# Optimization experiments

Measured on AMD Instinct MI355X. Metric: run time of the kernel, lower is better.

The kernel has to match this reference:

```python
import jax, jax.numpy as jnp
import numpy as np

H = 2048
NH = 16
DH = H // NH
EPS = 1e-05


def setup_inputs() -> dict:
    key = jax.random.key(0)
    ks = jax.random.split(key, 12)
    B, S, A = 4, 2048, 512
    s = 1.0 / np.sqrt(H)
    inp = {
        "hidden_states": jax.random.normal(ks[0], (B, S, H), jnp.float32),
        "audio_tokens": jax.random.normal(ks[1], (B, A, H), jnp.float32),
        "attention_mask": jax.random.randint(ks[2], (B, A), 0, 2).astype(jnp.float32),
        "Wq": jax.random.normal(ks[3], (H, H), jnp.float32) * s,
        "bq": jnp.zeros((H,), jnp.float32),
        "Wk": jax.random.normal(ks[4], (H, H), jnp.float32) * s,
        "bk": jnp.zeros((H,), jnp.float32),
        "Wv": jax.random.normal(ks[5], (H, H), jnp.float32) * s,
        "bv": jnp.zeros((H,), jnp.float32),
        "Wo": jax.random.normal(ks[6], (H, H), jnp.float32) * s,
        "bo": jnp.zeros((H,), jnp.float32),
        "gamma": jnp.ones((H,), jnp.float32),
        "beta": jnp.zeros((H,), jnp.float32),
    }
    return inp


def reference(hidden_states, audio_tokens, attention_mask,
              Wq, bq, Wk, bk, Wv, bv, Wo, bo, gamma, beta):
    B, S, _ = hidden_states.shape
    A = audio_tokens.shape[1]
    # projections (weights stored [in, out])
    q = (hidden_states @ Wq + bq).reshape(B, S, NH, DH)
    k = (audio_tokens @ Wk + bk).reshape(B, A, NH, DH)
    v = (audio_tokens @ Wv + bv).reshape(B, A, NH, DH)
    # scores: [B, NH, S, A]
    scores = jnp.einsum('bqhd,bkhd->bhqk', q, k) / np.sqrt(DH)
    scores = scores + attention_mask[:, None, None, :] * -10000.0
    probs = jax.nn.softmax(scores, axis=-1)
    # context: [B, S, NH, DH] -> [B, S, H]
    ctx = jnp.einsum('bhqk,bkhd->bqhd', probs, v).reshape(B, S, H)
    out = ctx @ Wo + bo
    # residual + LayerNorm
    x = out + hidden_states
    mu = jnp.mean(x, axis=-1, keepdims=True)
    var = jnp.mean(jnp.square(x - mu), axis=-1, keepdims=True)
    return (x - mu) * jax.lax.rsqrt(var + EPS) * gamma + beta
```

## Files before the change

### kernel.cpp

```cpp
#include <hip/hip_runtime.h>

#define HDIM 2048
#define NHEAD 16
#define DHEAD 128
#define BATCH 4
#define SEQ 2048
#define AUD 512

typedef unsigned short u16;
typedef unsigned int u32;
typedef __bf16 bf16_t;
typedef bf16_t bf16x8 __attribute__((ext_vector_type(8)));
typedef short short8 __attribute__((ext_vector_type(8)));
typedef float f32x4 __attribute__((ext_vector_type(4)));

typedef const __attribute__((address_space(1))) u32 gas_u32;
typedef __attribute__((address_space(3))) u32 las_u32;

__device__ __forceinline__ float b2f(u16 h) {
  union { u32 u; float f; } v; v.u = ((u32)h) << 16; return v.f;
}
__device__ __forceinline__ u16 f2b(float f) {
  union { float f; u32 u; } v; v.f = f;
  u32 r = (v.u + 0x7FFFu + ((v.u >> 16) & 1u)) >> 16;
  return (u16)r;
}

__global__ __launch_bounds__(256) void cvt2_k(const float* __restrict__ s0,
                                              u16* __restrict__ d0, int n0,
                                              const float* __restrict__ s1,
                                              u16* __restrict__ d1, int n1) {
  int i = blockIdx.x * 256 + threadIdx.x;
  const float* src; u16* dst; int j;
  if (i < n0) { src = s0; dst = d0; j = i; }
  else { j = i - n0; if (j >= n1) return; src = s1; dst = d1; }
  const float4* s4 = (const float4*)src;
  float4 a = s4[2 * j], b = s4[2 * j + 1];
  short8 o;
  o[0] = (short)f2b(a.x); o[1] = (short)f2b(a.y);
  o[2] = (short)f2b(a.z); o[3] = (short)f2b(a.w);
  o[4] = (short)f2b(b.x); o[5] = (short)f2b(b.y);
  o[6] = (short)f2b(b.z); o[7] = (short)f2b(b.w);
  *(short8*)(dst + (size_t)j * 8) = o;
}

__global__ __launch_bounds__(256) void transpose4_k(
    const float* __restrict__ Wq, const float* __restrict__ Wk,
    const float* __restrict__ Wv, const float* __restrict__ Wo,
    u16* __restrict__ dst4) {
  const float* src = (blockIdx.z == 0) ? Wq
                   : (blockIdx.z == 1) ? Wk
                   : (blockIdx.z == 2) ? Wv : Wo;
  u16* dst = dst4 + (size_t)blockIdx.z * HDIM * HDIM;
  __shared__ float tile[32][33];
  int tx = threadIdx.x, ty = threadIdx.y;
  int x = blockIdx.x * 32 + tx;
  int y0 = blockIdx.y * 32;
#pragma unroll
  for (int j = 0; j < 32; j += 8)
    tile[ty + j][tx] = src[(size_t)(y0 + ty + j) * HDIM + x];
  __syncthreads();
  int x2 = y0 + tx;
  int y2 = blockIdx.x * 32;
#pragma unroll
  for (int j = 0; j < 32; j += 8)
    dst[(size_t)(y2 + ty + j) * HDIM + x2] = f2b(tile[tx][ty + j]);
}

__global__ __launch_bounds__(256) void gemm_bt(
    const u16* __restrict__ A, int lda,
    const u16* __restrict__ Bt, int ldb,
    void* __restrict__ Cv, int ldc,
    const float* __restrict__ bias, float alpha, int M, int N, int K, int cmode) {
  __shared__ u16 As[128 * 32];
  __shared__ u16 Bs[128 * 32];

  int lane = threadIdx.x & 63;
  int wave = threadIdx.x >> 6;
  int gdx = gridDim.x;
  int id = blockIdx.y * gdx + blockIdx.x;
  int cpx = (gdx * gridDim.y) >> 3;
  int sid = (id & 7) * cpx + (id >> 3);
  int m0 = (sid / gdx) * 128;
  int n0 = (sid % gdx) * 128;
  int wm = (wave & 1) * 64;
  int wn = (wave >> 1) * 64;
  int row16 = lane & 15;
  int quad = lane >> 4;

  int sr = (lane >> 2);
  int sc = (lane & 3) * 8;

  f32x4 acc[4][4];
#pragma unroll
  for (int i = 0; i < 4; i++)
#pragma unroll
    for (int j = 0; j < 4; j++) acc[i][j] = (f32x4){0.f, 0.f, 0.f, 0.f};

  for (int k0 = 0; k0 < K; k0 += 32) {
#pragma unroll
    for (int t = 0; t < 2; t++) {
      int chunk = wave * 2 + t;
      int r = chunk * 16 + sr;
      const u16* ga = A + (size_t)(m0 + r) * lda + k0 + sc;
      const u16* gb = Bt + (size_t)(n0 + r) * ldb + k0 + sc;
      __builtin_amdgcn_global_load_lds((gas_u32*)ga, (las_u32*)(As + chunk * 512), 16, 0, 0);
      __builtin_amdgcn_global_load_lds((gas_u32*)gb, (las_u32*)(Bs + chunk * 512), 16, 0, 0);
    }
    __syncthreads();

    short8 af[4], bf[4];
#pragma unroll
    for (int mt = 0; mt < 4; mt++)
      af[mt] = *(const short8*)(As + (wm + mt * 16 + row16) * 32 + quad * 8);
#pragma unroll
    for (int nt = 0; nt < 4; nt++)
      bf[nt] = *(const short8*)(Bs + (wn + nt * 16 + row16) * 32 + quad * 8);
#pragma unroll
    for (int mt = 0; mt < 4; mt++)
#pragma unroll
      for (int nt = 0; nt < 4; nt++)
        acc[mt][nt] = __builtin_amdgcn_mfma_f32_16x16x32_bf16(
            __builtin_bit_cast(bf16x8, af[mt]), __builtin_bit_cast(bf16x8, bf[nt]),
            acc[mt][nt], 0, 0, 0);
    __syncthreads();
  }

#pragma unroll
  for (int nt = 0; nt < 4; nt++) {
    int nn = n0 + wn + nt * 16 + row16;
    float bv = bias ? bias[nn] : 0.f;
#pragma unroll
    for (int mt = 0; mt < 4; mt++) {
#pragma unroll
      for (int r = 0; r < 4; r++) {
        int mm = m0 + wm + mt * 16 + quad * 4 + r;
        float val = (acc[mt][nt][r] + bv) * alpha;
        if (cmode == 2) {
          ((float*)Cv)[(size_t)mm * ldc + nn] = val;
        } else if (cmode == 1) {
          int bb = mm >> 9, aa = mm & 511;
          int hh = nn >> 7, dd = nn & 127;
          ((u16*)Cv)[((size_t)((bb * 16 + hh) * 128 + dd)) * 512 + aa] = f2b(val);
        } else {
          ((u16*)Cv)[(size_t)mm * ldc + nn] = f2b(val);
        }
      }
    }
  }
}

__global__ __launch_bounds__(512, 2) void gemm_ring(
    const u16* __restrict__ A, int lda,
    const u16* __restrict__ Bt, int ldb,
    void* __restrict__ Cv, int ldc,
    const float* __restrict__ bias, float alpha, int K, int cmode) {
  __shared__ u16 As[3][256 * 64];
  __shared__ u16 Bs[3][128 * 64];

  int tid = threadIdx.x;
  int lane = tid & 63, wave = tid >> 6;
  int wr = wave >> 1, wc = wave & 1;
  int row16 = lane & 15, quad = lane >> 4;
  int swr = (row16 & 7) << 3;

  int gdx = gridDim.x;
  int id = blockIdx.y * gdx + blockIdx.x;
  int cpx = (gdx * gridDim.y) >> 3;
  int sid = (id & 7) * cpx + (id >> 3);
  int n0 = (sid % gdx) * 128;
  int m0 = (sid / gdx) * 256;

  f32x4 acc[4][4];
#pragma unroll
  for (int i = 0; i < 4; i++)
#pragma unroll
    for (int j = 0; j < 4; j++) acc[i][j] = (f32x4){0.f, 0.f, 0.f, 0.f};

  auto stage = [&](int slot, int k0) {
#pragma unroll
    for (int l = 0; l < 4; l++) {
      int d = l * 512 + tid;
      int row = d >> 3;
      int csw = ((d & 7) ^ (row & 7)) << 3;
      __builtin_amdgcn_global_load_lds(
          (gas_u32*)(A + (size_t)(m0 + row) * lda + k0 + csw),
          (las_u32*)(&As[slot][d * 8]), 16, 0, 0);
    }
#pragma unroll
    for (int l = 0; l < 2; l++) {
      int d = l * 512 + tid;
      int row = d >> 3;
      int csw = ((d & 7) ^ (row & 7)) << 3;
      __builtin_amdgcn_global_load_lds(
          (gas_u32*)(Bt + (size_t)(n0 + row) * ldb + k0 + csw),
          (las_u32*)(&Bs[slot][d * 8]), 16, 0, 0);
    }
  };

  auto compute = [&](int slot) {
#pragma unroll
    for (int kk = 0; kk < 2; kk++) {
      int cof = (kk * 32 + quad * 8) ^ swr;
      short8 af[4], bfr[4];
#pragma unroll
      for (int mi = 0; mi < 4; mi++)
        af[mi] = *(const short8*)(&As[slot][(wr * 64 + mi * 16 + row16) * 64 + cof]);
#pragma unroll
      for (int ni = 0; ni < 4; ni++)
        bfr[ni] = *(const short8*)(&Bs[slot][(wc * 64 + ni * 16 + row16) * 64 + cof]);
#pragma unroll
      for (int mi = 0; mi < 4; mi++)
#pragma unroll
        for (int ni = 0; ni < 4; ni++)
          acc[mi][ni] = __builtin_amdgcn_mfma_f32_16x16x32_bf16(
              __builtin_bit_cast(bf16x8, af[mi]), __builtin_bit_cast(bf16x8, bfr[ni]),
              acc[mi][ni], 0, 0, 0);
    }
  };

  int NT = K >> 6;
  stage(0, 0);
  stage(1, 64);
  asm volatile("s_waitcnt vmcnt(6)" ::: "memory");
  __builtin_amdgcn_s_barrier();

  int slot = 0;
  for (int kt = 0; kt < NT; ++kt) {
    int s2 = slot + 2; if (s2 >= 3) s2 -= 3;
    if (kt + 2 < NT) stage(s2, (kt + 2) << 6);
    compute(slot);
    if (kt + 2 < NT) {
      asm volatile("s_waitcnt vmcnt(6) lgkmcnt(0)" ::: "memory");
    } else {
      asm volatile("s_waitcnt vmcnt(0) lgkmcnt(0)" ::: "memory");
    }
    __builtin_amdgcn_s_barrier();
    slot++; if (slot >= 3) slot -= 3;
  }

#pragma unroll
  for (int ni = 0; ni < 4; ni++) {
    int nn = n0 + wc * 64 + ni * 16 + row16;
    float bv = bias ? bias[nn] : 0.f;
#pragma unroll
    for (int mi = 0; mi < 4; mi++) {
#pragma unroll
      for (int r = 0; r < 4; r++) {
        int mm = m0 + wr * 64 + mi * 16 + quad * 4 + r;
        float val = (acc[mi][ni][r] + bv) * alpha;
        if (cmode == 2) ((float*)Cv)[(size_t)mm * ldc + nn] = val;
        else            ((u16*)Cv)[(size_t)mm * ldc + nn] = f2b(val);
      }
    }
  }
}

__global__ __launch_bounds__(256) void flash_k(
    const u16* __restrict__ Q, const u16* __restrict__ K,
    const u16* __restrict__ Vt, const float* __restrict__ mask,
    u16* __restrict__ Ctx) {
  __shared__ u16 KP[128 * 128];
  __shared__ u16 Vs[128 * 128];

  int bh = blockIdx.y, b = bh >> 4, h = bh & 15;
  int q0 = blockIdx.x * 128;
  int lane = threadIdx.x & 63, wave = threadIdx.x >> 6;
  int row16 = lane & 15, quad = lane >> 4;
  int wq = wave * 32;
  int swr = (row16 & 7) << 3;

  const u16* qbase = Q + ((size_t)(b * SEQ + q0)) * HDIM + h * DHEAD;
  const u16* kbase = K + ((size_t)b * AUD) * HDIM + h * DHEAD;
  const u16* vbase = Vt + ((size_t)(b * NHEAD + h)) * DHEAD * AUD;
  const float* mp = mask + b * AUD;

  short8 qf[2][4];
#pragma unroll
  for (int mt = 0; mt < 2; mt++)
#pragma unroll
    for (int ks = 0; ks < 4; ks++)
      qf[mt][ks] = *(const short8*)(qbase + (size_t)(wq + mt * 16 + row16) * HDIM +
                                    ks * 32 + quad * 8);

  f32x4 oacc[2][8];
  float lacc[2][4];
#pragma unroll
  for (int mt = 0; mt < 2; mt++) {
#pragma unroll
    for (int nt = 0; nt < 8; nt++) oacc[mt][nt] = (f32x4){0.f, 0.f, 0.f, 0.f};
#pragma unroll
    for (int r = 0; r < 4; r++) lacc[mt][r] = 0.f;
  }

  int sl = (lane >> 4);
  int scol = (lane & 15) * 8;

  for (int kt = 0; kt < 4; kt++) {
#pragma unroll
    for (int t = 0; t < 8; t++) {
      int c = wave * 8 + t;
      int r = c * 4 + sl;
      int csw = scol ^ ((r & 7) << 3);
      __builtin_amdgcn_global_load_lds(
          (gas_u32*)(kbase + (size_t)(kt * 128 + r) * HDIM + csw),
          (las_u32*)(KP + c * 512), 16, 0, 0);
      __builtin_amdgcn_global_load_lds(
          (gas_u32*)(vbase + (size_t)r * AUD + kt * 128 + csw),
          (las_u32*)(Vs + c * 512), 16, 0, 0);
    }
    __syncthreads();

    f32x4 sacc[2][8];
#pragma unroll
    for (int mt = 0; mt < 2; mt++)
#pragma unroll
      for (int nt = 0; nt < 8; nt++) sacc[mt][nt] = (f32x4){0.f, 0.f, 0.f, 0.f};
#pragma unroll
    for (int ks = 0; ks < 4; ks++) {
      short8 bf[8];
      int cofs = (ks * 32 + quad * 8) ^ swr;
#pragma unroll
      for (int nt = 0; nt < 8; nt++)
        bf[nt] = *(const short8*)(KP + (nt * 16 + row16) * 128 + cofs);
#pragma unroll
      for (int mt = 0; mt < 2; mt++)
#pragma unroll
        for (int nt = 0; nt < 8; nt++)
          sacc[mt][nt] = __builtin_amdgcn_mfma_f32_16x16x32_bf16(
              __builtin_bit_cast(bf16x8, qf[mt][ks]), __builtin_bit_cast(bf16x8, bf[nt]),
              sacc[mt][nt], 0, 0, 0);
    }

#pragma unroll
    for (int nt = 0; nt < 8; nt++) {
      float mval = mp[kt * 128 + nt * 16 + row16] * (-10000.0f);
#pragma unroll
      for (int mt = 0; mt < 2; mt++)
#pragma unroll
        for (int r = 0; r < 4; r++) {
          float e = __expf(sacc[mt][nt][r] + mval);
          sacc[mt][nt][r] = e;
          lacc[mt][r] += e;
        }
    }
    __syncthreads();

#pragma unroll
    for (int mt = 0; mt < 2; mt++)
#pragma unroll
      for (int nt = 0; nt < 8; nt++)
#pragma unroll
        for (int r = 0; r < 4; r++) {
          int prow = wq + mt * 16 + quad * 4 + r;
          KP[prow * 128 + ((nt * 16 + row16) ^ ((prow & 7) << 3))] =
              f2b(sacc[mt][nt][r]);
        }
    __syncthreads();

#pragma unroll
    for (int ks = 0; ks < 4; ks++) {
      short8 af[2], bf[8];
      int cofs = (ks * 32 + quad * 8) ^ swr;
#pragma unroll
      for (int mt = 0; mt < 2; mt++)
        af[mt] = *(const short8*)(KP + (wq + mt * 16 + row16) * 128 + cofs);
#pragma unroll
      for (int nt = 0; nt < 8; nt++)
        bf[nt] = *(const short8*)(Vs + (nt * 16 + row16) * 128 + cofs);
#pragma unroll
      for (int mt = 0; mt < 2; mt++)
#pragma unroll
        for (int nt = 0; nt < 8; nt++)
          oacc[mt][nt] = __builtin_amdgcn_mfma_f32_16x16x32_bf16(
              __builtin_bit_cast(bf16x8, af[mt]), __builtin_bit_cast(bf16x8, bf[nt]),
              oacc[mt][nt], 0, 0, 0);
    }
    __syncthreads();
  }

#pragma unroll
  for (int mt = 0; mt < 2; mt++)
#pragma unroll
    for (int r = 0; r < 4; r++) {
      float s = lacc[mt][r];
      for (int off = 1; off < 16; off <<= 1) s += __shfl_xor(s, off, 64);
      lacc[mt][r] = 1.0f / s;
    }

  u16* cb = Ctx + ((size_t)(b * SEQ + q0 + wq)) * HDIM + h * DHEAD;
#pragma unroll
  for (int mt = 0; mt < 2; mt++)
#pragma unroll
    for (int nt = 0; nt < 8; nt++)
#pragma unroll
      for (int r = 0; r < 4; r++)
        cb[(size_t)(mt * 16 + quad * 4 + r) * HDIM + nt * 16 + row16] =
            f2b(oacc[mt][nt][r] * lacc[mt][r]);
}

__global__ __launch_bounds__(256) void ln_k(const float* O,
                                            const float* __restrict__ hs,
                                            const float* __restrict__ gamma,
                                            const float* __restrict__ beta,
                                            float* out) {
  size_t rowoff = (size_t)blockIdx.x * HDIM;
  float x[8], sum = 0.f, sq = 0.f;
#pragma unroll
  for (int i = 0; i < 8; i++) {
    int idx = threadIdx.x + 256 * i;
    float v = O[rowoff + idx] + hs[rowoff + idx];
    x[i] = v;
    sum += v;
    sq += v * v;
  }
  for (int off = 32; off; off >>= 1) {
    sum += __shfl_xor(sum, off, 64);
    sq += __shfl_xor(sq, off, 64);
  }
  __shared__ float red[8];
  int wave = threadIdx.x >> 6, lane = threadIdx.x & 63;
  if (lane == 0) { red[wave] = sum; red[4 + wave] = sq; }
  __syncthreads();
  sum = red[0] + red[1] + red[2] + red[3];
  sq = red[4] + red[5] + red[6] + red[7];
  float mu = sum * (1.0f / HDIM);
  float var = sq * (1.0f / HDIM) - mu * mu;
  float inv = rsqrtf(var + 1e-5f);
#pragma unroll
  for (int i = 0; i < 8; i++) {
    int idx = threadIdx.x + 256 * i;
    out[rowoff + idx] = (x[i] - mu) * inv * gamma[idx] + beta[idx];
  }
}

extern "C" void kernel_launch(void* const* d_in, const int* in_sizes, int n_in,
                              void* d_out, int out_size, void* d_ws, size_t ws_size,
                              hipStream_t stream) {
  (void)in_sizes; (void)n_in; (void)out_size; (void)ws_size;
  const float* hs   = (const float*)d_in[0];
  const float* at   = (const float*)d_in[1];
  const float* mask = (const float*)d_in[2];
  const float* Wq = (const float*)d_in[3];  const float* bq = (const float*)d_in[4];
  const float* Wk = (const float*)d_in[5];  const float* bk = (const float*)d_in[6];
  const float* Wv = (const float*)d_in[7];  const float* bv = (const float*)d_in[8];
  const float* Wo = (const float*)d_in[9];  const float* bo = (const float*)d_in[10];
  const float* gamma = (const float*)d_in[11];
  const float* beta  = (const float*)d_in[12];
  float* out = (float*)d_out;
  u16* ws = (u16*)d_ws;

  u16* hsb = ws;
  u16* atb = ws + 16777216;
  u16* wT4 = ws + 20971520;
  u16* Q   = ws + 37748736;
  u16* Kb  = ws + 54525952;
  u16* Vt  = ws + 58720256;
  u16* Ctx = ws + 62914560;
  u16* wTq = wT4;
  u16* wTk = wT4 + 4194304;
  u16* wTv = wT4 + 8388608;
  u16* wTo = wT4 + 12582912;

  cvt2_k<<<10240, 256, 0, stream>>>(hs, hsb, 2097152, at, atb, 524288);
  transpose4_k<<<dim3(64, 64, 4), dim3(32, 8), 0, stream>>>(Wq, Wk, Wv, Wo, wT4);

  const float qscale = 0.08838834764831845f;

  gemm_ring<<<dim3(16, 32), 512, 0, stream>>>(hsb, HDIM, wTq, HDIM, Q, HDIM,
                                              bq, qscale, 2048, 0);
  gemm_bt<<<dim3(16, 16), 256, 0, stream>>>(atb, HDIM, wTk, HDIM, Kb, HDIM,
                                            bk, 1.0f, 2048, 2048, 2048, 0);
  gemm_bt<<<dim3(16, 16), 256, 0, stream>>>(atb, HDIM, wTv, HDIM, Vt, HDIM,
                                            bv, 1.0f, 2048, 2048, 2048, 1);

  flash_k<<<dim3(SEQ / 128, BATCH * NHEAD), 256, 0, stream>>>(Q, Kb, Vt, mask, Ctx);

  gemm_ring<<<dim3(16, 32), 512, 0, stream>>>(Ctx, HDIM, wTo, HDIM, out, HDIM,
                                              bo, 1.0f, 2048, 2);
  ln_k<<<8192, 256, 0, stream>>>(out, hs, gamma, beta, out);
}
```

Baseline: 611.0 us.

## Retile ring GEMM to K=32 stages, fuse K/V GEMMs, swizzle flash blocks

The ring GEMM now uses 32-wide K stages with smaller LDS buffers and a launch bound of four blocks per CU. Its loop issues the fragment loads first, then the prefetch, then a barrier, and runs the MFMAs at raised priority. The K and V projections are merged into one launch over a concatenated weight (wTk followed by wTv, N=4096), with a new cmode that writes K row-major and V transposed. The flash kernel remaps block IDs for XCD-aware scheduling and drops one __syncthreads between writing P to LDS and reading it. That barrier removal risks a race, because each wave reads KP rows only it wrote, but Vs reuse may depend on it.

```diff
diff --git a/kernel.cpp b/kernel.cpp
--- a/kernel.cpp
+++ b/kernel.cpp
@@ -71,7 +71,8 @@
     const u16* __restrict__ A, int lda,
     const u16* __restrict__ Bt, int ldb,
     void* __restrict__ Cv, int ldc,
-    const float* __restrict__ bias, float alpha, int M, int N, int K, int cmode) {
+    const float* __restrict__ bias, const float* __restrict__ bias2,
+    float alpha, int M, int N, int K, int cmode) {
   __shared__ u16 As[128 * 32];
   __shared__ u16 Bs[128 * 32];
 
@@ -129,7 +130,9 @@
 #pragma unroll
   for (int nt = 0; nt < 4; nt++) {
     int nn = n0 + wn + nt * 16 + row16;
-    float bv = bias ? bias[nn] : 0.f;
+    float bv;
+    if (cmode == 3) bv = (nn < 2048) ? bias[nn] : bias2[nn - 2048];
+    else            bv = bias ? bias[nn] : 0.f;
 #pragma unroll
     for (int mt = 0; mt < 4; mt++) {
 #pragma unroll
@@ -138,10 +141,16 @@
         float val = (acc[mt][nt][r] + bv) * alpha;
         if (cmode == 2) {
           ((float*)Cv)[(size_t)mm * ldc + nn] = val;
-        } else if (cmode == 1) {
-          int bb = mm >> 9, aa = mm & 511;
-          int hh = nn >> 7, dd = nn & 127;
-          ((u16*)Cv)[((size_t)((bb * 16 + hh) * 128 + dd)) * 512 + aa] = f2b(val);
+        } else if (cmode == 3) {
+          if (nn < 2048) {
+            ((u16*)Cv)[(size_t)mm * ldc + nn] = f2b(val);
+          } else {
+            int nn2 = nn - 2048;
+            int bb = mm >> 9, aa = mm & 511;
+            int hh = nn2 >> 7, dd = nn2 & 127;
+            ((u16*)Cv + 4194304)[((size_t)((bb * 16 + hh) * 128 + dd)) * 512 + aa] =
+                f2b(val);
+          }
         } else {
           ((u16*)Cv)[(size_t)mm * ldc + nn] = f2b(val);
         }
@@ -150,19 +159,19 @@
   }
 }
 
-__global__ __launch_bounds__(512, 2) void gemm_ring(
+__global__ __launch_bounds__(512, 4) void gemm_ring8(
     const u16* __restrict__ A, int lda,
     const u16* __restrict__ Bt, int ldb,
     void* __restrict__ Cv, int ldc,
     const float* __restrict__ bias, float alpha, int K, int cmode) {
-  __shared__ u16 As[3][256 * 64];
-  __shared__ u16 Bs[3][128 * 64];
+  __shared__ u16 As[3][256 * 32];
+  __shared__ u16 Bs[3][128 * 32];
 
   int tid = threadIdx.x;
   int lane = tid & 63, wave = tid >> 6;
   int wr = wave >> 1, wc = wave & 1;
   int row16 = lane & 15, quad = lane >> 4;
-  int swr = (row16 & 7) << 3;
+  int cofs = (quad * 8) ^ (((row16 >> 1) & 3) << 3);
 
   int gdx = gridDim.x;
   int id = blockIdx.y * gdx + blockIdx.x;
@@ -171,6 +180,9 @@
   int n0 = (sid % gdx) * 128;
   int m0 = (sid / gdx) * 256;
 
+  int r0 = tid >> 2;
+  int c0 = ((tid & 3) ^ ((r0 >> 1) & 3)) * 8;
+
   f32x4 acc[4][4];
 #pragma unroll
   for (int i = 0; i < 4; i++)
@@ -179,64 +191,53 @@
 
   auto stage = [&](int slot, int k0) {
 #pragma unroll
-    for (int l = 0; l < 4; l++) {
-      int d = l * 512 + tid;
-      int row = d >> 3;
-      int csw = ((d & 7) ^ (row & 7)) << 3;
+    for (int l = 0; l < 2; l++) {
+      int row = l * 128 + r0;
       __builtin_amdgcn_global_load_lds(
-          (gas_u32*)(A + (size_t)(m0 + row) * lda + k0 + csw),
-          (las_u32*)(&As[slot][d * 8]), 16, 0, 0);
-    }
-#pragma unroll
-    for (int l = 0; l < 2; l++) {
-      int d = l * 512 + tid;
-      int row = d >> 3;
-      int csw = ((d & 7) ^ (row & 7)) << 3;
-      __builtin_amdgcn_global_load_lds(
-          (gas_u32*)(Bt + (size_t)(n0 + row) * ldb + k0 + csw),
-          (las_u32*)(&Bs[slot][d * 8]), 16, 0, 0);
-    }
+          (gas_u32*)(A + (size_t)(m0 + row) * lda + k0 + c0),
+          (las_u32*)(&As[slot][(l * 512 + tid) * 8]), 16, 0, 0);
+    }
+    __builtin_amdgcn_global_load_lds(
+        (gas_u32*)(Bt + (size_t)(n0 + r0) * ldb + k0 + c0),
+        (las_u32*)(&Bs[slot][(size_t)tid * 8]), 16, 0, 0);
   };
 
-  auto compute = [&](int slot) {
-#pragma unroll
-    for (int kk = 0; kk < 2; kk++) {
-      int cof = (kk * 32 + quad * 8) ^ swr;
-      short8 af[4], bfr[4];
-#pragma unroll
-      for (int mi = 0; mi < 4; mi++)
-        af[mi] = *(const short8*)(&As[slot][(wr * 64 + mi * 16 + row16) * 64 + cof]);
-#pragma unroll
-      for (int ni = 0; ni < 4; ni++)
-        bfr[ni] = *(const short8*)(&Bs[slot][(wc * 64 + ni * 16 + row16) * 64 + cof]);
-#pragma unroll
-      for (int mi = 0; mi < 4; mi++)
-#pragma unroll
-        for (int ni = 0; ni < 4; ni++)
-          acc[mi][ni] = __builtin_amdgcn_mfma_f32_16x16x32_bf16(
-              __builtin_bit_cast(bf16x8, af[mi]), __builtin_bit_cast(bf16x8, bfr[ni]),
-              acc[mi][ni], 0, 0, 0);
-    }
-  };
-
-  int NT = K >> 6;
+  int NT = K >> 5;
   stage(0, 0);
-  stage(1, 64);
-  asm volatile("s_waitcnt vmcnt(6)" ::: "memory");
+  stage(1, 32);
+  asm volatile("s_waitcnt vmcnt(3)" ::: "memory");
   __builtin_amdgcn_s_barrier();
 
   int slot = 0;
   for (int kt = 0; kt < NT; ++kt) {
-    int s2 = slot + 2; if (s2 >= 3) s2 -= 3;
-    if (kt + 2 < NT) stage(s2, (kt + 2) << 6);
-    compute(slot);
-    if (kt + 2 < NT) {
-      asm volatile("s_waitcnt vmcnt(6) lgkmcnt(0)" ::: "memory");
-    } else {
-      asm volatile("s_waitcnt vmcnt(0) lgkmcnt(0)" ::: "memory");
-    }
+    int sp = (slot >= 1) ? slot - 1 : 2;
+    bool pf = (kt + 2) < NT;
+    const u16* as = &As[slot][0];
+    const u16* bs = &Bs[slot][0];
+
+    short8 af[4], bfr[4];
+#pragma unroll
+    for (int mi = 0; mi < 4; mi++)
+      af[mi] = *(const short8*)(as + (wr * 64 + mi * 16 + row16) * 32 + cofs);
+#pragma unroll
+    for (int ni = 0; ni < 4; ni++)
+      bfr[ni] = *(const short8*)(bs + (wc * 64 + ni * 16 + row16) * 32 + cofs);
+    if (pf) stage(sp, (kt + 2) << 5);
+    if (pf) { asm volatile("s_waitcnt vmcnt(3)" ::: "memory"); }
+    else    { asm volatile("s_waitcnt vmcnt(0)" ::: "memory"); }
     __builtin_amdgcn_s_barrier();
-    slot++; if (slot >= 3) slot -= 3;
+    asm volatile("s_waitcnt lgkmcnt(0)" ::: "memory");
+    __builtin_amdgcn_s_setprio(1);
+#pragma unroll
+    for (int mi = 0; mi < 4; mi++)
+#pragma unroll
+      for (int ni = 0; ni < 4; ni++)
+        acc[mi][ni] = __builtin_amdgcn_mfma_f32_16x16x32_bf16(
+            __builtin_bit_cast(bf16x8, af[mi]), __builtin_bit_cast(bf16x8, bfr[ni]),
+            acc[mi][ni], 0, 0, 0);
+    __builtin_amdgcn_s_setprio(0);
+    __builtin_amdgcn_s_barrier();
+    slot = (slot >= 2) ? 0 : slot + 1;
   }
 
 #pragma unroll
@@ -263,8 +264,12 @@
   __shared__ u16 KP[128 * 128];
   __shared__ u16 Vs[128 * 128];
 
-  int bh = blockIdx.y, b = bh >> 4, h = bh & 15;
-  int q0 = blockIdx.x * 128;
+  int id = blockIdx.y * gridDim.x + blockIdx.x;
+  int sid = (id & 7) * 128 + (id >> 3);
+  int qt = sid & 15, bh = sid >> 4;
+  int b = bh >> 4, h = bh & 15;
+  int q0 = qt * 128;
+
   int lane = threadIdx.x & 63, wave = threadIdx.x >> 6;
   int row16 = lane & 15, quad = lane >> 4;
   int wq = wave * 32;
@@ -356,7 +361,6 @@
           KP[prow * 128 + ((nt * 16 + row16) ^ ((prow & 7) << 3))] =
               f2b(sacc[mt][nt][r]);
         }
-    __syncthreads();
 
 #pragma unroll
     for (int ks = 0; ks < 4; ks++) {
@@ -459,7 +463,6 @@
   u16* Ctx = ws + 62914560;
   u16* wTq = wT4;
   u16* wTk = wT4 + 4194304;
-  u16* wTv = wT4 + 8388608;
   u16* wTo = wT4 + 12582912;
 
   cvt2_k<<<10240, 256, 0, stream>>>(hs, hsb, 2097152, at, atb, 524288);
@@ -467,16 +470,14 @@
 
   const float qscale = 0.08838834764831845f;
 
-  gemm_ring<<<dim3(16, 32), 512, 0, stream>>>(hsb, HDIM, wTq, HDIM, Q, HDIM,
-                                              bq, qscale, 2048, 0);
-  gemm_bt<<<dim3(16, 16), 256, 0, stream>>>(atb, HDIM, wTk, HDIM, Kb, HDIM,
-                                            bk, 1.0f, 2048, 2048, 2048, 0);
-  gemm_bt<<<dim3(16, 16), 256, 0, stream>>>(atb, HDIM, wTv, HDIM, Vt, HDIM,
-                                            bv, 1.0f, 2048, 2048, 2048, 1);
+  gemm_ring8<<<dim3(16, 32), 512, 0, stream>>>(hsb, HDIM, wTq, HDIM, Q, HDIM,
+                                               bq, qscale, 2048, 0);
+  gemm_bt<<<dim3(32, 16), 256, 0, stream>>>(atb, HDIM, wTk, HDIM, Kb, 2048,
+                                            bk, bv, 1.0f, 2048, 4096, 2048, 3);
 
   flash_k<<<dim3(SEQ / 128, BATCH * NHEAD), 256, 0, stream>>>(Q, Kb, Vt, mask, Ctx);
 
-  gemm_ring<<<dim3(16, 32), 512, 0, stream>>>(Ctx, HDIM, wTo, HDIM, out, HDIM,
-                                              bo, 1.0f, 2048, 2);
+  gemm_ring8<<<dim3(16, 32), 512, 0, stream>>>(Ctx, HDIM, wTo, HDIM, out, HDIM,
+                                               bo, 1.0f, 2048, 2);
   ln_k<<<8192, 256, 0, stream>>>(out, hs, gamma, beta, out);
 }
```

Result: faster. 514.3 us (-15.8%).
